# Optimization experiments

Measured on AMD Instinct MI355X. Metric: run time of the kernel, lower is better.

## Reference

```python
import jax, jax.numpy as jnp
import numpy as np

ALPHA = 0.9
N_NODES = 100000
N_EDGES = 3200000
F_IN = 256
UNITS = 256
INIT_DIM = 3


def setup_inputs() -> dict:
    key = jax.random.key(0)
    k = jax.random.split(key, 7)
    x = jax.random.normal(k[0], (N_NODES, F_IN), dtype=jnp.float32)
    x_initial = jax.random.normal(k[1], (N_NODES, INIT_DIM), dtype=jnp.float32)
    adj_row = jax.random.randint(k[2], (N_EDGES,), 0, N_NODES, dtype=jnp.int32)
    adj_col = jax.random.randint(k[3], (N_EDGES,), 0, N_NODES, dtype=jnp.int32)
    # normalized-adjacency-like small positive edge weights
    adj_val = jax.random.uniform(k[4], (N_EDGES,), dtype=jnp.float32) * (1.0 / 32.0)
    w_init = jax.random.normal(k[5], (INIT_DIM, F_IN), dtype=jnp.float32) * 0.05
    w_x = jax.random.normal(k[6], (F_IN, UNITS), dtype=jnp.float32) * 0.05
    return {"x": x, "x_initial": x_initial, "adj_row": adj_row, "adj_col": adj_col,
            "adj_val": adj_val, "w_init": w_init, "w_x": w_x}


def reference(x, x_initial, adj_row, adj_col, adj_val, w_init, w_x):
    # sparse adj @ x : gather source-node features, weight by edge value,
    # scatter-add into destination rows (COO SpMM)
    agg = jax.ops.segment_sum(adj_val[:, None] * x[adj_col], adj_row,
                              num_segments=x.shape[0])  # [N, F]
    # alpha-blend with projection of initial features
    h = ALPHA * agg + (1.0 - ALPHA) * (x_initial @ w_init)  # [N, F]
    # dense projection + activation
    return jax.nn.relu(h @ w_x)  # [N, units]
```

## Files before the change

### kernel.cpp

```cpp
#include <hip/hip_runtime.h>


static constexpr int   NN = 100000;
static constexpr int   NE = 3200000;
static constexpr float W_ALPHA = 0.9f;
static constexpr float W_OMA   = 0.1f;

typedef float f32x4 __attribute__((ext_vector_type(4)));

__device__ __forceinline__ unsigned int bf16_rtn(float f) {
    unsigned int b = __float_as_uint(f);
    return (b + 0x7FFFu + ((b >> 16) & 1u)) >> 16;
}
__device__ __forceinline__ float bf16_dec(unsigned short u) {
    return __uint_as_float((unsigned int)u << 16);
}

__global__ void k_hist(const int* __restrict__ row, int* __restrict__ counts, int E) {
    int i = blockIdx.x * blockDim.x + threadIdx.x;
    int stride = gridDim.x * blockDim.x;
    for (; i < E; i += stride) atomicAdd(&counts[row[i]], 1);
}

__global__ void k_scan_block(const int* __restrict__ counts, int* __restrict__ off,
                             int* __restrict__ btot, int N) {
    __shared__ int s_w[17];
    const int tid = threadIdx.x, lane = tid & 63, wid = tid >> 6;
    const int i = blockIdx.x * 1024 + tid;
    int v = (i < N) ? counts[i] : 0;
    int x = v;
    #pragma unroll
    for (int d = 1; d < 64; d <<= 1) {
        int t = __shfl_up(x, d);
        if (lane >= d) x += t;
    }
    if (lane == 63) s_w[wid] = x;
    __syncthreads();
    if (wid == 0) {
        int wv = (lane < 16) ? s_w[lane] : 0;
        int wx = wv;
        #pragma unroll
        for (int d = 1; d < 16; d <<= 1) {
            int t = __shfl_up(wx, d);
            if (lane >= d) wx += t;
        }
        if (lane < 16) s_w[lane] = wx - wv;
        if (lane == 15) s_w[16] = wx;
    }
    __syncthreads();
    if (i < N) off[i] = s_w[wid] + (x - v);
    if (tid == 0) btot[blockIdx.x] = s_w[16];
}

__global__ void k_scan_tops(const int* __restrict__ btot, int* __restrict__ boff,
                            int NB, int* __restrict__ total_out) {
    __shared__ int s[128];
    const int tid = threadIdx.x;
    int v = (tid < NB) ? btot[tid] : 0;
    s[tid] = v;
    __syncthreads();
    for (int d = 1; d < 128; d <<= 1) {
        int t = (tid >= d) ? s[tid - d] : 0;
        __syncthreads();
        s[tid] += t;
        __syncthreads();
    }
    if (tid < NB) boff[tid] = s[tid] - v;
    if (tid == NB - 1) *total_out = s[tid];
}

__global__ void k_scan_add(int* __restrict__ off, int* __restrict__ cursor,
                           const int* __restrict__ boff, int N) {
    const int i = blockIdx.x * 1024 + threadIdx.x;
    if (i < N) {
        int o = off[i] + boff[blockIdx.x];
        off[i] = o;
        cursor[i] = o;
    }
}

__global__ void k_scatter_pack(const int* __restrict__ row, const int* __restrict__ col,
                               const float* __restrict__ val, int* __restrict__ cursor,
                               int2* __restrict__ e_pack, int E) {
    int i = blockIdx.x * blockDim.x + threadIdx.x;
    int stride = gridDim.x * blockDim.x;
    for (; i < E; i += stride) {
        int r = row[i];
        int p = atomicAdd(&cursor[r], 1);
        e_pack[p] = make_int2(col[i], __float_as_int(val[i]));
    }
}

__global__ void k_wc(const float* __restrict__ wi, const float* __restrict__ wx,
                     float* __restrict__ wc) {
    const int n = threadIdx.x;
    float a0 = 0.f, a1 = 0.f, a2 = 0.f;
    for (int k = 0; k < 256; ++k) {
        float w = wx[k * 256 + n];
        a0 += wi[k] * w;
        a1 += wi[256 + k] * w;
        a2 += wi[512 + k] * w;
    }
    wc[n]       = W_OMA * a0;
    wc[256 + n] = W_OMA * a1;
    wc[512 + n] = W_OMA * a2;
}

__global__ void k_spmm_fused(const unsigned short* __restrict__ y, const float* __restrict__ xi,
                             const float* __restrict__ wc,
                             const int* __restrict__ off, const int2* __restrict__ e_pack,
                             float* __restrict__ out, int N) {
    const int lane = threadIdx.x & 63;
    const int wid  = threadIdx.x >> 6;
    const int r    = blockIdx.x * 4 + wid;
    if (r >= N) return;
    const int beg = off[r], end = off[r + 1];
    const ushort4* __restrict__ y4 = (const ushort4*)y;
    f32x4 acc0 = {0.f, 0.f, 0.f, 0.f};
    f32x4 acc1 = {0.f, 0.f, 0.f, 0.f};
    f32x4 acc2 = {0.f, 0.f, 0.f, 0.f};
    f32x4 acc3 = {0.f, 0.f, 0.f, 0.f};
    int k = beg;
    for (; k + 3 < end; k += 4) {
        int2 e0 = e_pack[k],     e1 = e_pack[k + 1];
        int2 e2 = e_pack[k + 2], e3 = e_pack[k + 3];
        ushort4 a = y4[(size_t)e0.x * 64 + lane];
        ushort4 b = y4[(size_t)e1.x * 64 + lane];
        ushort4 c = y4[(size_t)e2.x * 64 + lane];
        ushort4 d = y4[(size_t)e3.x * 64 + lane];
        float v0 = __int_as_float(e0.y), v1 = __int_as_float(e1.y);
        float v2 = __int_as_float(e2.y), v3 = __int_as_float(e3.y);
        f32x4 fa = {bf16_dec(a.x), bf16_dec(a.y), bf16_dec(a.z), bf16_dec(a.w)};
        f32x4 fb = {bf16_dec(b.x), bf16_dec(b.y), bf16_dec(b.z), bf16_dec(b.w)};
        f32x4 fc = {bf16_dec(c.x), bf16_dec(c.y), bf16_dec(c.z), bf16_dec(c.w)};
        f32x4 fd = {bf16_dec(d.x), bf16_dec(d.y), bf16_dec(d.z), bf16_dec(d.w)};
        acc0 += v0 * fa;
        acc1 += v1 * fb;
        acc2 += v2 * fc;
        acc3 += v3 * fd;
    }
    for (; k < end; ++k) {
        int2 e = e_pack[k];
        ushort4 a = y4[(size_t)e.x * 64 + lane];
        float v = __int_as_float(e.y);
        f32x4 fa = {bf16_dec(a.x), bf16_dec(a.y), bf16_dec(a.z), bf16_dec(a.w)};
        acc0 += v * fa;
    }
    acc0 += acc1 + acc2 + acc3;
    float i0 = xi[r * 3 + 0], i1 = xi[r * 3 + 1], i2 = xi[r * 3 + 2];
    const f32x4* __restrict__ wc4 = (const f32x4*)wc;
    f32x4 b0 = wc4[lane], b1 = wc4[64 + lane], b2 = wc4[128 + lane];
    f32x4 hv = acc0 + i0 * b0 + i1 * b1 + i2 * b2;
    hv.x = fmaxf(hv.x, 0.f);
    hv.y = fmaxf(hv.y, 0.f);
    hv.z = fmaxf(hv.z, 0.f);
    hv.w = fmaxf(hv.w, 0.f);
    __builtin_nontemporal_store(hv, (f32x4*)out + (size_t)r * 64 + lane);
}

#define FMA4(A, S) { A.x += (S) * w.x; A.y += (S) * w.y; A.z += (S) * w.z; A.w += (S) * w.w; }
__global__ __launch_bounds__(256, 4)
void k_gemm_y(const float* __restrict__ xin, const float* __restrict__ wx,
              unsigned short* __restrict__ y, int M) {
    __shared__ float wsh[32][256];
    __shared__ float hsT[32][64];
    const int tid  = threadIdx.x;
    const int rg   = tid >> 6;
    const int lane = tid & 63;
    const int row0 = blockIdx.x * 64;

    float4 acc[16];
    #pragma unroll
    for (int i = 0; i < 16; ++i) acc[i] = make_float4(0.f, 0.f, 0.f, 0.f);

    for (int kk = 0; kk < 256; kk += 32) {
        {
            int k  = tid >> 3;
            int c0 = (tid & 7) * 4;
            const float4* src = (const float4*)(wx + (size_t)(kk + k) * 256);
            #pragma unroll
            for (int c8 = 0; c8 < 8; ++c8) {
                float4 v = src[(c0 >> 2) + c8 * 8];
                *(float4*)&wsh[k][c0 + c8 * 32] = v;
            }
        }
        {
            int rr = tid >> 3;
            int k4 = (tid & 7) * 4;
            #pragma unroll
            for (int p = 0; p < 2; ++p) {
                int r = row0 + rr + p * 32;
                f32x4 v = {0.f, 0.f, 0.f, 0.f};
                if (r < M) v = __builtin_nontemporal_load(
                    (const f32x4*)(xin + (size_t)r * 256 + kk + k4));
                hsT[k4 + 0][rr + p * 32] = v.x;
                hsT[k4 + 1][rr + p * 32] = v.y;
                hsT[k4 + 2][rr + p * 32] = v.z;
                hsT[k4 + 3][rr + p * 32] = v.w;
            }
        }
        __syncthreads();
        #pragma unroll
        for (int k = 0; k < 32; ++k) {
            float4 w  = *(const float4*)&wsh[k][lane * 4];
            float4 h0 = *(const float4*)&hsT[k][rg * 16 + 0];
            float4 h1 = *(const float4*)&hsT[k][rg * 16 + 4];
            float4 h2 = *(const float4*)&hsT[k][rg * 16 + 8];
            float4 h3 = *(const float4*)&hsT[k][rg * 16 + 12];
            FMA4(acc[0],  h0.x) FMA4(acc[1],  h0.y) FMA4(acc[2],  h0.z) FMA4(acc[3],  h0.w)
            FMA4(acc[4],  h1.x) FMA4(acc[5],  h1.y) FMA4(acc[6],  h1.z) FMA4(acc[7],  h1.w)
            FMA4(acc[8],  h2.x) FMA4(acc[9],  h2.y) FMA4(acc[10], h2.z) FMA4(acc[11], h2.w)
            FMA4(acc[12], h3.x) FMA4(acc[13], h3.y) FMA4(acc[14], h3.z) FMA4(acc[15], h3.w)
        }
        __syncthreads();
    }
    #pragma unroll
    for (int i = 0; i < 16; ++i) {
        int r = row0 + rg * 16 + i;
        if (r < M) {
            unsigned int u0 = bf16_rtn(W_ALPHA * acc[i].x);
            unsigned int u1 = bf16_rtn(W_ALPHA * acc[i].y);
            unsigned int u2 = bf16_rtn(W_ALPHA * acc[i].z);
            unsigned int u3 = bf16_rtn(W_ALPHA * acc[i].w);
            uint2 pk = make_uint2(u0 | (u1 << 16), u2 | (u3 << 16));
            *(uint2*)(y + (size_t)r * 256 + lane * 4) = pk;
        }
    }
}

__global__ void k_scatter(const int* __restrict__ row, const int* __restrict__ col,
                          const float* __restrict__ val, int* __restrict__ cursor,
                          int* __restrict__ e_col, float* __restrict__ e_val, int E) {
    int i = blockIdx.x * blockDim.x + threadIdx.x;
    int stride = gridDim.x * blockDim.x;
    for (; i < E; i += stride) {
        int r = row[i];
        int p = atomicAdd(&cursor[r], 1);
        e_col[p] = col[i];
        e_val[p] = val[i];
    }
}

__global__ void k_spmm(const float* __restrict__ x, const float* __restrict__ xi,
                       const float* __restrict__ w_init,
                       const int* __restrict__ off, const int* __restrict__ e_col,
                       const float* __restrict__ e_val,
                       float* __restrict__ h, int N) {
    const int lane = threadIdx.x & 63;
    const int wid  = threadIdx.x >> 6;
    const int r    = blockIdx.x * 4 + wid;
    if (r >= N) return;
    const int beg = off[r], end = off[r + 1];
    const float4* __restrict__ x4 = (const float4*)x;
    float4 acc0 = make_float4(0.f, 0.f, 0.f, 0.f);
    float4 acc1 = make_float4(0.f, 0.f, 0.f, 0.f);
    int k = beg;
    for (; k + 1 < end; k += 2) {
        int   c0 = e_col[k],     c1 = e_col[k + 1];
        float v0 = e_val[k],     v1 = e_val[k + 1];
        float4 a = x4[(size_t)c0 * 64 + lane];
        float4 b = x4[(size_t)c1 * 64 + lane];
        acc0.x += v0 * a.x; acc0.y += v0 * a.y; acc0.z += v0 * a.z; acc0.w += v0 * a.w;
        acc1.x += v1 * b.x; acc1.y += v1 * b.y; acc1.z += v1 * b.z; acc1.w += v1 * b.w;
    }
    if (k < end) {
        int   c = e_col[k];
        float v = e_val[k];
        float4 a = x4[(size_t)c * 64 + lane];
        acc0.x += v * a.x; acc0.y += v * a.y; acc0.z += v * a.z; acc0.w += v * a.w;
    }
    acc0.x += acc1.x; acc0.y += acc1.y; acc0.z += acc1.z; acc0.w += acc1.w;
    float i0 = xi[r * 3 + 0], i1 = xi[r * 3 + 1], i2 = xi[r * 3 + 2];
    const float4* __restrict__ w4 = (const float4*)w_init;
    float4 w0 = w4[lane], w1 = w4[64 + lane], w2 = w4[128 + lane];
    float4 hv;
    hv.x = W_ALPHA * acc0.x + W_OMA * (i0 * w0.x + i1 * w1.x + i2 * w2.x);
    hv.y = W_ALPHA * acc0.y + W_OMA * (i0 * w0.y + i1 * w1.y + i2 * w2.y);
    hv.z = W_ALPHA * acc0.z + W_OMA * (i0 * w0.z + i1 * w1.z + i2 * w2.z);
    hv.w = W_ALPHA * acc0.w + W_OMA * (i0 * w0.w + i1 * w1.w + i2 * w2.w);
    ((float4*)h)[(size_t)r * 64 + lane] = hv;
}

__global__ void k_blend_init(const float* __restrict__ xi, const float* __restrict__ w_init,
                             float* __restrict__ h, int N) {
    const int lane = threadIdx.x & 63;
    const int wid  = threadIdx.x >> 6;
    const int r    = blockIdx.x * 4 + wid;
    if (r >= N) return;
    float i0 = xi[r * 3 + 0], i1 = xi[r * 3 + 1], i2 = xi[r * 3 + 2];
    const float4* __restrict__ w4 = (const float4*)w_init;
    float4 w0 = w4[lane], w1 = w4[64 + lane], w2 = w4[128 + lane];
    float4 hv;
    hv.x = W_OMA * (i0 * w0.x + i1 * w1.x + i2 * w2.x);
    hv.y = W_OMA * (i0 * w0.y + i1 * w1.y + i2 * w2.y);
    hv.z = W_OMA * (i0 * w0.z + i1 * w1.z + i2 * w2.z);
    hv.w = W_OMA * (i0 * w0.w + i1 * w1.w + i2 * w2.w);
    ((float4*)h)[(size_t)r * 64 + lane] = hv;
}

__global__ void k_spmm_atomic(const float* __restrict__ x,
                              const int* __restrict__ row, const int* __restrict__ col,
                              const float* __restrict__ val,
                              float* __restrict__ h, int E) {
    const int lane = threadIdx.x & 63;
    const int wid  = threadIdx.x >> 6;
    int e = blockIdx.x * 4 + wid;
    const int estride = gridDim.x * 4;
    const float4* __restrict__ x4 = (const float4*)x;
    for (; e < E; e += estride) {
        int r = row[e], c = col[e];
        float v = W_ALPHA * val[e];
        float4 xv = x4[(size_t)c * 64 + lane];
        float* dst = h + (size_t)r * 256 + lane * 4;
        atomicAdd(dst + 0, v * xv.x);
        atomicAdd(dst + 1, v * xv.y);
        atomicAdd(dst + 2, v * xv.z);
        atomicAdd(dst + 3, v * xv.w);
    }
}

__global__ __launch_bounds__(256, 4)
void k_gemm_relu(float* __restrict__ hout, const float* __restrict__ wx, int M) {
    __shared__ float wsh[32][256];
    __shared__ float hsT[32][64];
    const int tid  = threadIdx.x;
    const int rg   = tid >> 6;
    const int lane = tid & 63;
    const int row0 = blockIdx.x * 64;

    float4 acc[16];
    #pragma unroll
    for (int i = 0; i < 16; ++i) acc[i] = make_float4(0.f, 0.f, 0.f, 0.f);

    for (int kk = 0; kk < 256; kk += 32) {
        {
            int k  = tid >> 3;
            int c0 = (tid & 7) * 4;
            const float4* src = (const float4*)(wx + (size_t)(kk + k) * 256);
            #pragma unroll
            for (int c8 = 0; c8 < 8; ++c8) {
                float4 v = src[(c0 >> 2) + c8 * 8];
                *(float4*)&wsh[k][c0 + c8 * 32] = v;
            }
        }
        {
            int rr = tid >> 3;
            int k4 = (tid & 7) * 4;
            #pragma unroll
            for (int p = 0; p < 2; ++p) {
                int r = row0 + rr + p * 32;
                float4 v = make_float4(0.f, 0.f, 0.f, 0.f);
                if (r < M) v = *(const float4*)(hout + (size_t)r * 256 + kk + k4);
                hsT[k4 + 0][rr + p * 32] = v.x;
                hsT[k4 + 1][rr + p * 32] = v.y;
                hsT[k4 + 2][rr + p * 32] = v.z;
                hsT[k4 + 3][rr + p * 32] = v.w;
            }
        }
        __syncthreads();
        #pragma unroll
        for (int k = 0; k < 32; ++k) {
            float4 w  = *(const float4*)&wsh[k][lane * 4];
            float4 h0 = *(const float4*)&hsT[k][rg * 16 + 0];
            float4 h1 = *(const float4*)&hsT[k][rg * 16 + 4];
            float4 h2 = *(const float4*)&hsT[k][rg * 16 + 8];
            float4 h3 = *(const float4*)&hsT[k][rg * 16 + 12];
            FMA4(acc[0],  h0.x) FMA4(acc[1],  h0.y) FMA4(acc[2],  h0.z) FMA4(acc[3],  h0.w)
            FMA4(acc[4],  h1.x) FMA4(acc[5],  h1.y) FMA4(acc[6],  h1.z) FMA4(acc[7],  h1.w)
            FMA4(acc[8],  h2.x) FMA4(acc[9],  h2.y) FMA4(acc[10], h2.z) FMA4(acc[11], h2.w)
            FMA4(acc[12], h3.x) FMA4(acc[13], h3.y) FMA4(acc[14], h3.z) FMA4(acc[15], h3.w)
        }
        __syncthreads();
    }
    #pragma unroll
    for (int i = 0; i < 16; ++i) {
        int r = row0 + rg * 16 + i;
        if (r < M) {
            float4 v;
            v.x = fmaxf(acc[i].x, 0.f);
            v.y = fmaxf(acc[i].y, 0.f);
            v.z = fmaxf(acc[i].z, 0.f);
            v.w = fmaxf(acc[i].w, 0.f);
            *(float4*)(hout + (size_t)r * 256 + lane * 4) = v;
        }
    }
}

static inline size_t alignup(size_t v, size_t a) { return (v + a - 1) & ~(a - 1); }

extern "C" void kernel_launch(void* const* d_in, const int* in_sizes, int n_in,
                              void* d_out, int out_size, void* d_ws, size_t ws_size,
                              hipStream_t stream) {
    const float* x       = (const float*)d_in[0];
    const float* x_init  = (const float*)d_in[1];
    const int*   adj_row = (const int*)d_in[2];
    const int*   adj_col = (const int*)d_in[3];
    const float* adj_val = (const float*)d_in[4];
    const float* w_init  = (const float*)d_in[5];
    const float* w_x     = (const float*)d_in[6];
    float* out = (float*)d_out;

    const int NB = (NN + 1023) / 1024;

    const size_t sz_ybf    = alignup((size_t)NN * 256 * 2, 256);
    const size_t sz_counts = alignup((size_t)NN * 4, 256);
    const size_t sz_off    = alignup((size_t)(NN + 1) * 4, 256);
    const size_t sz_cursor = alignup((size_t)NN * 4, 256);
    const size_t sz_epack  = alignup((size_t)NE * 8, 256);
    const size_t sz_ecol   = alignup((size_t)NE * 4, 256);
    const size_t sz_eval   = alignup((size_t)NE * 4, 256);
    const size_t sz_btot   = alignup((size_t)NB * 4, 256);
    const size_t sz_wc     = alignup((size_t)3 * 256 * 4, 256);
    const size_t need_full = sz_counts + sz_off + sz_cursor + 2 * sz_btot
                           + sz_epack + sz_ybf + sz_wc;
    const size_t need_csr  = sz_counts + sz_off + sz_cursor + 2 * sz_btot
                           + sz_ecol + sz_eval;

    if (ws_size >= need_full) {
        char* ws = (char*)d_ws;
        unsigned short* y = (unsigned short*)ws;  ws += sz_ybf;
        float* wc     = (float*)ws;  ws += sz_wc;
        int*   counts = (int*)ws;    ws += sz_counts;
        int*   off    = (int*)ws;    ws += sz_off;
        int*   cursor = (int*)ws;    ws += sz_cursor;
        int*   btot   = (int*)ws;    ws += sz_btot;
        int*   boff   = (int*)ws;    ws += sz_btot;
        int2*  e_pack = (int2*)ws;   ws += sz_epack;

        (void)hipMemsetAsync(counts, 0, (size_t)NN * 4, stream);
        k_hist<<<2048, 256, 0, stream>>>(adj_row, counts, NE);
        k_scan_block<<<NB, 1024, 0, stream>>>(counts, off, btot, NN);
        k_scan_tops<<<1, 128, 0, stream>>>(btot, boff, NB, off + NN);
        k_scan_add<<<NB, 1024, 0, stream>>>(off, cursor, boff, NN);
        k_scatter_pack<<<2048, 256, 0, stream>>>(adj_row, adj_col, adj_val, cursor, e_pack, NE);
        k_gemm_y<<<(NN + 63) / 64, 256, 0, stream>>>(x, w_x, y, NN);
        k_wc<<<1, 256, 0, stream>>>(w_init, w_x, wc);
        k_spmm_fused<<<NN / 4, 256, 0, stream>>>(y, x_init, wc, off, e_pack, out, NN);
    } else if (ws_size >= need_csr) {
        char* ws = (char*)d_ws;
        int*   counts = (int*)ws;    ws += sz_counts;
        int*   off    = (int*)ws;    ws += sz_off;
        int*   cursor = (int*)ws;    ws += sz_cursor;
        int*   btot   = (int*)ws;    ws += sz_btot;
        int*   boff   = (int*)ws;    ws += sz_btot;
        int*   e_col  = (int*)ws;    ws += sz_ecol;
        float* e_val  = (float*)ws;  ws += sz_eval;

        (void)hipMemsetAsync(counts, 0, (size_t)NN * 4, stream);
        k_hist<<<2048, 256, 0, stream>>>(adj_row, counts, NE);
        k_scan_block<<<NB, 1024, 0, stream>>>(counts, off, btot, NN);
        k_scan_tops<<<1, 128, 0, stream>>>(btot, boff, NB, off + NN);
        k_scan_add<<<NB, 1024, 0, stream>>>(off, cursor, boff, NN);
        k_scatter<<<2048, 256, 0, stream>>>(adj_row, adj_col, adj_val, cursor, e_col, e_val, NE);
        k_spmm<<<NN / 4, 256, 0, stream>>>(x, x_init, w_init, off, e_col, e_val, out, NN);
        k_gemm_relu<<<(NN + 63) / 64, 256, 0, stream>>>(out, w_x, NN);
    } else {
        k_blend_init<<<NN / 4, 256, 0, stream>>>(x_init, w_init, out, NN);
        k_spmm_atomic<<<8192, 256, 0, stream>>>(x, adj_row, adj_col, adj_val, out, NE);
        k_gemm_relu<<<(NN + 63) / 64, 256, 0, stream>>>(out, w_x, NN);
    }
}
```

Before: 985.3 us.

## Partition histogram and scatter by destination-row range per block group

The histogram and CSR scatter kernels now assign each block one of 8 row-range partitions. A block scans the whole edge list but only performs atomics and writes for rows in its own range. The aim is locality: atomics on the count/cursor arrays and the packed edge writes from a group of blocks fall in a narrower address range and may stay in L2/MALL. The cost is that the row array is read 8 times (with nontemporal loads). Separately, the SpMM edge-list reads switch to nontemporal loads to avoid polluting cache with streaming data.

```diff
diff --git a/kernel.cpp b/kernel.cpp
--- a/kernel.cpp
+++ b/kernel.cpp
@@ -3,10 +3,12 @@
 
 static constexpr int   NN = 100000;
 static constexpr int   NE = 3200000;
+static constexpr int   NPART = 8;
 static constexpr float W_ALPHA = 0.9f;
 static constexpr float W_OMA   = 0.1f;
 
 typedef float f32x4 __attribute__((ext_vector_type(4)));
+typedef int   i32x2 __attribute__((ext_vector_type(2)));
 
 __device__ __forceinline__ unsigned int bf16_rtn(float f) {
     unsigned int b = __float_as_uint(f);
@@ -14,6 +16,18 @@
 }
 __device__ __forceinline__ float bf16_dec(unsigned short u) {
     return __uint_as_float((unsigned int)u << 16);
+}
+
+__global__ void k_hist_part(const int* __restrict__ row, int* __restrict__ counts, int E) {
+    const int part = blockIdx.x & (NPART - 1);
+    const int rlo  = part * (NN / NPART);
+    const int rhi  = rlo + (NN / NPART);
+    int i = (blockIdx.x >> 3) * blockDim.x + threadIdx.x;
+    const int stride = (gridDim.x >> 3) * blockDim.x;
+    for (; i < E; i += stride) {
+        int r = __builtin_nontemporal_load(row + i);
+        if (r >= rlo && r < rhi) atomicAdd(&counts[r], 1);
+    }
 }
 
 __global__ void k_hist(const int* __restrict__ row, int* __restrict__ counts, int E) {
@@ -79,15 +93,35 @@
     }
 }
 
-__global__ void k_scatter_pack(const int* __restrict__ row, const int* __restrict__ col,
+__global__ void k_scatter_part(const int* __restrict__ row, const int* __restrict__ col,
                                const float* __restrict__ val, int* __restrict__ cursor,
                                int2* __restrict__ e_pack, int E) {
+    const int part = blockIdx.x & (NPART - 1);
+    const int rlo  = part * (NN / NPART);
+    const int rhi  = rlo + (NN / NPART);
+    int i = (blockIdx.x >> 3) * blockDim.x + threadIdx.x;
+    const int stride = (gridDim.x >> 3) * blockDim.x;
+    for (; i < E; i += stride) {
+        int r = __builtin_nontemporal_load(row + i);
+        if (r >= rlo && r < rhi) {
+            int c = __builtin_nontemporal_load(col + i);
+            float v = __builtin_nontemporal_load(val + i);
+            int p = atomicAdd(&cursor[r], 1);
+            e_pack[p] = make_int2(c, __float_as_int(v));
+        }
+    }
+}
+
+__global__ void k_scatter(const int* __restrict__ row, const int* __restrict__ col,
+                          const float* __restrict__ val, int* __restrict__ cursor,
+                          int* __restrict__ e_col, float* __restrict__ e_val, int E) {
     int i = blockIdx.x * blockDim.x + threadIdx.x;
     int stride = gridDim.x * blockDim.x;
     for (; i < E; i += stride) {
         int r = row[i];
         int p = atomicAdd(&cursor[r], 1);
-        e_pack[p] = make_int2(col[i], __float_as_int(val[i]));
+        e_col[p] = col[i];
+        e_val[p] = val[i];
     }
 }
 
@@ -116,14 +150,17 @@
     if (r >= N) return;
     const int beg = off[r], end = off[r + 1];
     const ushort4* __restrict__ y4 = (const ushort4*)y;
+    const i32x2* __restrict__ ep = (const i32x2*)e_pack;
     f32x4 acc0 = {0.f, 0.f, 0.f, 0.f};
     f32x4 acc1 = {0.f, 0.f, 0.f, 0.f};
     f32x4 acc2 = {0.f, 0.f, 0.f, 0.f};
     f32x4 acc3 = {0.f, 0.f, 0.f, 0.f};
     int k = beg;
     for (; k + 3 < end; k += 4) {
-        int2 e0 = e_pack[k],     e1 = e_pack[k + 1];
-        int2 e2 = e_pack[k + 2], e3 = e_pack[k + 3];
+        i32x2 e0 = __builtin_nontemporal_load(ep + k);
+        i32x2 e1 = __builtin_nontemporal_load(ep + k + 1);
+        i32x2 e2 = __builtin_nontemporal_load(ep + k + 2);
+        i32x2 e3 = __builtin_nontemporal_load(ep + k + 3);
         ushort4 a = y4[(size_t)e0.x * 64 + lane];
         ushort4 b = y4[(size_t)e1.x * 64 + lane];
         ushort4 c = y4[(size_t)e2.x * 64 + lane];
@@ -140,7 +177,7 @@
         acc3 += v3 * fd;
     }
     for (; k < end; ++k) {
-        int2 e = e_pack[k];
+        i32x2 e = __builtin_nontemporal_load(ep + k);
         ushort4 a = y4[(size_t)e.x * 64 + lane];
         float v = __int_as_float(e.y);
         f32x4 fa = {bf16_dec(a.x), bf16_dec(a.y), bf16_dec(a.z), bf16_dec(a.w)};
@@ -225,19 +262,6 @@
             uint2 pk = make_uint2(u0 | (u1 << 16), u2 | (u3 << 16));
             *(uint2*)(y + (size_t)r * 256 + lane * 4) = pk;
         }
-    }
-}
-
-__global__ void k_scatter(const int* __restrict__ row, const int* __restrict__ col,
-                          const float* __restrict__ val, int* __restrict__ cursor,
-                          int* __restrict__ e_col, float* __restrict__ e_val, int E) {
-    int i = blockIdx.x * blockDim.x + threadIdx.x;
-    int stride = gridDim.x * blockDim.x;
-    for (; i < E; i += stride) {
-        int r = row[i];
-        int p = atomicAdd(&cursor[r], 1);
-        e_col[p] = col[i];
-        e_val[p] = val[i];
     }
 }
 
@@ -428,11 +452,11 @@
         int2*  e_pack = (int2*)ws;   ws += sz_epack;
 
         (void)hipMemsetAsync(counts, 0, (size_t)NN * 4, stream);
-        k_hist<<<2048, 256, 0, stream>>>(adj_row, counts, NE);
+        k_hist_part<<<2048, 256, 0, stream>>>(adj_row, counts, NE);
         k_scan_block<<<NB, 1024, 0, stream>>>(counts, off, btot, NN);
         k_scan_tops<<<1, 128, 0, stream>>>(btot, boff, NB, off + NN);
         k_scan_add<<<NB, 1024, 0, stream>>>(off, cursor, boff, NN);
-        k_scatter_pack<<<2048, 256, 0, stream>>>(adj_row, adj_col, adj_val, cursor, e_pack, NE);
+        k_scatter_part<<<2048, 256, 0, stream>>>(adj_row, adj_col, adj_val, cursor, e_pack, NE);
         k_gemm_y<<<(NN + 63) / 64, 256, 0, stream>>>(x, w_x, y, NN);
         k_wc<<<1, 256, 0, stream>>>(w_init, w_x, wc);
         k_spmm_fused<<<NN / 4, 256, 0, stream>>>(y, x_init, wc, off, e_pack, out, NN);
```

Result: faster. 901.7 us (-8.5%).
